# Kernel tuning notes

Measured on AMD Instinct MI355X. Metric: run time of the kernel, lower is better.

The kernel has to match this reference:

```python
import jax, jax.numpy as jnp
import numpy as np

D = 1024
H = 16
HD = D // H


def setup_inputs() -> dict:
    key = jax.random.key(0)
    ks = jax.random.split(key, 9)
    s = 1.0 / np.sqrt(D)
    return {
        "x": jax.random.normal(ks[0], (2, 2048, D), dtype=jnp.float32),
        "Wq": jax.random.normal(ks[1], (D, D), dtype=jnp.float32) * s,
        "bq": jax.random.normal(ks[2], (D,), dtype=jnp.float32) * s,
        "Wk": jax.random.normal(ks[3], (D, D), dtype=jnp.float32) * s,
        "bk": jax.random.normal(ks[4], (D,), dtype=jnp.float32) * s,
        "Wv": jax.random.normal(ks[5], (D, D), dtype=jnp.float32) * s,
        "bv": jax.random.normal(ks[6], (D,), dtype=jnp.float32) * s,
        "Wo": jax.random.normal(ks[7], (D, D), dtype=jnp.float32) * s,
        "bo": jax.random.normal(ks[8], (D,), dtype=jnp.float32) * s,
    }


def reference(x, Wq, bq, Wk, bk, Wv, bv, Wo, bo):
    B, S, _ = x.shape
    # Linear projections (torch Linear: y = x @ W.T + b)
    q = x @ Wq.T + bq
    k = x @ Wk.T + bk
    v = x @ Wv.T + bv
    # split heads: [B, S, H, HD] -> [B, H, S, HD]
    q = q.reshape(B, S, H, HD).transpose(0, 2, 1, 3)
    k = k.reshape(B, S, H, HD).transpose(0, 2, 1, 3)
    v = v.reshape(B, S, H, HD).transpose(0, 2, 1, 3)
    scale = 1.0 / jnp.sqrt(jnp.float32(HD))
    scores = jnp.einsum("bhqd,bhkd->bhqk", q, k) * scale  # [B,H,S,S]
    attn = jax.nn.softmax(scores, axis=-1)
    ctx = jnp.einsum("bhqk,bhkd->bhqd", attn, v)  # [B,H,S,HD]
    ctx = ctx.transpose(0, 2, 1, 3).reshape(B, S, D)
    out = ctx @ Wo.T + bo
    return out, attn
```

## Files before the change

### kernel.cpp

```cpp
#include <hip/hip_runtime.h>

#define S_LEN 2048
#define NH 16
#define HDIM 64
#define DMODEL 1024
#define NTOK 4096

typedef __attribute__((ext_vector_type(8))) short bf16x8;
typedef __attribute__((ext_vector_type(4))) float f32x4;

__device__ __forceinline__ unsigned short f2bf(float f) {
  union { float f; unsigned int u; } a; a.f = f;
  unsigned int u = a.u;
  u += 0x7FFFu + ((u >> 16) & 1u);
  return (unsigned short)(u >> 16);
}

__device__ __forceinline__ void gld_lds16(const unsigned short* g, unsigned short* l) {
  auto gp = (const __attribute__((address_space(1))) unsigned short*)(g);
  auto lp = (__attribute__((address_space(3))) unsigned short*)(l);
  __builtin_amdgcn_global_load_lds(gp, lp, 16, 0, 0);
}

__global__ __launch_bounds__(256) void cvt_kernel(const float* __restrict__ s,
                                                  unsigned short* __restrict__ d, int n) {
  int i = (blockIdx.x * 256 + threadIdx.x) * 4;
  if (i >= n) return;
  float4 v = *(const float4*)(s + i);
  ushort4 o;
  o.x = f2bf(v.x); o.y = f2bf(v.y); o.z = f2bf(v.z); o.w = f2bf(v.w);
  *(ushort4*)(d + i) = o;
}

__device__ __forceinline__ void gemm_core_128(
    const unsigned short* __restrict__ A, const unsigned short* __restrict__ B,
    unsigned short* Al, unsigned short* Bl, int m0, int n0, int tid, f32x4 acc[4][4])
{
  const int lane = tid & 63;
  const int wm = ((tid >> 6) >> 1) * 64;
  const int wn = ((tid >> 6) & 1) * 64;
  const int l15 = lane & 15, quad = lane >> 4;
  const int row0 = tid >> 2, c8 = (tid & 3) * 8;
  for (int kk = 0; kk < DMODEL; kk += 32) {
    gld_lds16(A + (size_t)(m0 + row0) * DMODEL + kk + c8,      Al + tid * 8);
    gld_lds16(A + (size_t)(m0 + 64 + row0) * DMODEL + kk + c8, Al + (256 + tid) * 8);
    gld_lds16(B + (size_t)(n0 + row0) * DMODEL + kk + c8,      Bl + tid * 8);
    gld_lds16(B + (size_t)(n0 + 64 + row0) * DMODEL + kk + c8, Bl + (256 + tid) * 8);
    __syncthreads();
    bf16x8 af[4], bfr[4];
#pragma unroll
    for (int i = 0; i < 4; i++) {
      af[i]  = *(const bf16x8*)(Al + (wm + i * 16 + l15) * 32 + quad * 8);
      bfr[i] = *(const bf16x8*)(Bl + (wn + i * 16 + l15) * 32 + quad * 8);
    }
#pragma unroll
    for (int i = 0; i < 4; i++)
#pragma unroll
      for (int j = 0; j < 4; j++)
        acc[i][j] = __builtin_amdgcn_mfma_f32_16x16x32_bf16(af[i], bfr[j], acc[i][j], 0, 0, 0);
    __syncthreads();
  }
}

__global__ __launch_bounds__(256) void gemm_qkv(
    const unsigned short* __restrict__ xb,
    const unsigned short* __restrict__ wq, const unsigned short* __restrict__ wk,
    const unsigned short* __restrict__ wv,
    const float* __restrict__ bq, const float* __restrict__ bk, const float* __restrict__ bv,
    unsigned short* __restrict__ q_ws, unsigned short* __restrict__ k_ws,
    unsigned short* __restrict__ vT_ws)
{
  __shared__ unsigned short Al[128 * 32];
  __shared__ unsigned short Bl[128 * 32];
  const int which = blockIdx.z;
  const unsigned short* W = which == 0 ? wq : (which == 1 ? wk : wv);
  const float* bias = which == 0 ? bq : (which == 1 ? bk : bv);
  const int m0 = blockIdx.y * 128, n0 = blockIdx.x * 128;
  const int tid = threadIdx.x, lane = tid & 63;
  const int wm = ((tid >> 6) >> 1) * 64, wn = ((tid >> 6) & 1) * 64;
  const int l15 = lane & 15, quad = lane >> 4;
  f32x4 acc[4][4] = {};
  gemm_core_128(xb, W, Al, Bl, m0, n0, tid, acc);
  const float scale = (which == 0) ? 0.125f : 1.0f;
  unsigned short* qk_dst = (which == 0) ? q_ws : k_ws;
#pragma unroll
  for (int j = 0; j < 4; j++) {
    const int n = n0 + wn + j * 16 + l15;
    const float bb = bias[n];
    const int h = n >> 6, d = n & 63;
#pragma unroll
    for (int i = 0; i < 4; i++)
#pragma unroll
      for (int r = 0; r < 4; r++) {
        const int m = m0 + wm + i * 16 + quad * 4 + r;
        const int b = m >> 11, s = m & 2047;
        const unsigned short o = f2bf((acc[i][j][r] + bb) * scale);
        if (which == 2)
          vT_ws[((size_t)(b * NH + h) * HDIM + d) * S_LEN + s] = o;
        else
          qk_dst[((size_t)(b * NH + h) * S_LEN + s) * HDIM + d] = o;
      }
  }
}

__global__ __launch_bounds__(256) void attn_fused(
    const unsigned short* __restrict__ q_ws, const unsigned short* __restrict__ k_ws,
    const unsigned short* __restrict__ vT_ws,
    float* __restrict__ attn_out, unsigned short* __restrict__ ctx_ws)
{
  __shared__ unsigned short p_lds[4][16 * 72];
  const int tid = threadIdx.x, lane = tid & 63, w = tid >> 6;
  const int l15 = lane & 15, quad = lane >> 4;
  const int bh = blockIdx.x >> 5, qtile = blockIdx.x & 31;
  const int qr0 = qtile * 64 + w * 16;

  const unsigned short* qp = q_ws + ((size_t)bh * S_LEN + qr0 + l15) * HDIM + quad * 8;
  bf16x8 aq0 = *(const bf16x8*)qp;
  bf16x8 aq1 = *(const bf16x8*)(qp + 32);

  const unsigned short* kbh = k_ws + (size_t)bh * S_LEN * HDIM;
  const unsigned short* vbh = vT_ws + (size_t)bh * HDIM * S_LEN;

  float lsum[4] = {0.f, 0.f, 0.f, 0.f};
  for (int kc = 0; kc < S_LEN; kc += 64) {
#pragma unroll
    for (int t = 0; t < 4; t++) {
      const unsigned short* kb = kbh + (size_t)(kc + t * 16 + l15) * HDIM + quad * 8;
      bf16x8 b0 = *(const bf16x8*)kb;
      bf16x8 b1 = *(const bf16x8*)(kb + 32);
      f32x4 s = {0.f, 0.f, 0.f, 0.f};
      s = __builtin_amdgcn_mfma_f32_16x16x32_bf16(aq0, b0, s, 0, 0, 0);
      s = __builtin_amdgcn_mfma_f32_16x16x32_bf16(aq1, b1, s, 0, 0, 0);
#pragma unroll
      for (int r = 0; r < 4; r++) lsum[r] += __expf(s[r]);
    }
  }
  float rinv[4];
#pragma unroll
  for (int r = 0; r < 4; r++) {
    float v = lsum[r];
    v += __shfl_xor(v, 1, 64);
    v += __shfl_xor(v, 2, 64);
    v += __shfl_xor(v, 4, 64);
    v += __shfl_xor(v, 8, 64);
    rinv[r] = 1.0f / v;
  }

  f32x4 cacc[4] = {};
  float* ab = attn_out + ((size_t)bh * S_LEN + qr0) * S_LEN;
  unsigned short* plw = &p_lds[w][0];
  for (int kc = 0; kc < S_LEN; kc += 64) {
#pragma unroll
    for (int t = 0; t < 4; t++) {
      const unsigned short* kb = kbh + (size_t)(kc + t * 16 + l15) * HDIM + quad * 8;
      bf16x8 b0 = *(const bf16x8*)kb;
      bf16x8 b1 = *(const bf16x8*)(kb + 32);
      f32x4 s = {0.f, 0.f, 0.f, 0.f};
      s = __builtin_amdgcn_mfma_f32_16x16x32_bf16(aq0, b0, s, 0, 0, 0);
      s = __builtin_amdgcn_mfma_f32_16x16x32_bf16(aq1, b1, s, 0, 0, 0);
#pragma unroll
      for (int r = 0; r < 4; r++) {
        const float p = __expf(s[r]) * rinv[r];
        ab[(size_t)(quad * 4 + r) * S_LEN + kc + t * 16 + l15] = p;
        plw[(quad * 4 + r) * 72 + t * 16 + l15] = f2bf(p);
      }
    }
    bf16x8 ap0 = *(const bf16x8*)(plw + l15 * 72 + quad * 8);
    bf16x8 ap1 = *(const bf16x8*)(plw + l15 * 72 + 32 + quad * 8);
#pragma unroll
    for (int dt = 0; dt < 4; dt++) {
      const unsigned short* vb = vbh + (size_t)(dt * 16 + l15) * S_LEN + kc + quad * 8;
      bf16x8 v0 = *(const bf16x8*)vb;
      bf16x8 v1 = *(const bf16x8*)(vb + 32);
      cacc[dt] = __builtin_amdgcn_mfma_f32_16x16x32_bf16(ap0, v0, cacc[dt], 0, 0, 0);
      cacc[dt] = __builtin_amdgcn_mfma_f32_16x16x32_bf16(ap1, v1, cacc[dt], 0, 0, 0);
    }
  }
  const int b = bh >> 4, h = bh & 15;
#pragma unroll
  for (int dt = 0; dt < 4; dt++)
#pragma unroll
    for (int r = 0; r < 4; r++) {
      const int s_ = qr0 + quad * 4 + r;
      const int d = dt * 16 + l15;
      ctx_ws[((size_t)(b * S_LEN + s_) * NH + h) * HDIM + d] = f2bf(cacc[dt][r]);
    }
}

__global__ __launch_bounds__(256) void gemm_out(
    const unsigned short* __restrict__ ctx, const unsigned short* __restrict__ wo,
    const float* __restrict__ bo, float* __restrict__ out)
{
  __shared__ unsigned short Al[128 * 32];
  __shared__ unsigned short Bl[128 * 32];
  const int m0 = blockIdx.y * 128, n0 = blockIdx.x * 128;
  const int tid = threadIdx.x, lane = tid & 63;
  const int wm = ((tid >> 6) >> 1) * 64, wn = ((tid >> 6) & 1) * 64;
  const int l15 = lane & 15, quad = lane >> 4;
  f32x4 acc[4][4] = {};
  gemm_core_128(ctx, wo, Al, Bl, m0, n0, tid, acc);
#pragma unroll
  for (int j = 0; j < 4; j++) {
    const int n = n0 + wn + j * 16 + l15;
    const float bb = bo[n];
#pragma unroll
    for (int i = 0; i < 4; i++)
#pragma unroll
      for (int r = 0; r < 4; r++) {
        const int m = m0 + wm + i * 16 + quad * 4 + r;
        out[(size_t)m * DMODEL + n] = acc[i][j][r] + bb;
      }
  }
}

extern "C" void kernel_launch(void* const* d_in, const int* in_sizes, int n_in,
                              void* d_out, int out_size, void* d_ws, size_t ws_size,
                              hipStream_t stream) {
  const float* x  = (const float*)d_in[0];
  const float* Wq = (const float*)d_in[1];
  const float* bq = (const float*)d_in[2];
  const float* Wk = (const float*)d_in[3];
  const float* bk = (const float*)d_in[4];
  const float* Wv = (const float*)d_in[5];
  const float* bv = (const float*)d_in[6];
  const float* Wo = (const float*)d_in[7];
  const float* bo = (const float*)d_in[8];

  const size_t MB = 1u << 20;
  char* ws = (char*)d_ws;
  unsigned short* xb     = (unsigned short*)(ws);
  unsigned short* wqb    = (unsigned short*)(ws + 8 * MB);
  unsigned short* wkb    = (unsigned short*)(ws + 10 * MB);
  unsigned short* wvb    = (unsigned short*)(ws + 12 * MB);
  unsigned short* wob    = (unsigned short*)(ws + 14 * MB);
  unsigned short* q_ws   = (unsigned short*)(ws + 16 * MB);
  unsigned short* k_ws   = (unsigned short*)(ws + 24 * MB);
  unsigned short* vT_ws  = (unsigned short*)(ws + 32 * MB);
  unsigned short* ctx_ws = (unsigned short*)(ws + 40 * MB);

  float* out_ptr  = (float*)d_out;
  float* attn_ptr = (float*)d_out + 4194304;

  cvt_kernel<<<4096, 256, 0, stream>>>(x,  xb,  4194304);
  cvt_kernel<<<1024, 256, 0, stream>>>(Wq, wqb, 1048576);
  cvt_kernel<<<1024, 256, 0, stream>>>(Wk, wkb, 1048576);
  cvt_kernel<<<1024, 256, 0, stream>>>(Wv, wvb, 1048576);
  cvt_kernel<<<1024, 256, 0, stream>>>(Wo, wob, 1048576);

  gemm_qkv<<<dim3(8, 32, 3), 256, 0, stream>>>(xb, wqb, wkb, wvb, bq, bk, bv,
                                               q_ws, k_ws, vT_ws);
  attn_fused<<<1024, 256, 0, stream>>>(q_ws, k_ws, vT_ws, attn_ptr, ctx_ws);
  gemm_out<<<dim3(8, 32, 1), 256, 0, stream>>>(ctx_ws, wob, bo, out_ptr);
}
```

Measured before the change: 1.015 ms.

## Split attention key range across warp pairs and vectorize probability stores

Each block now handles 32 query rows, with two waves per 16-row group, each covering half the key range. Row sums are combined through shared memory and partial context accumulators are reduced through LDS before the bf16 write. The MFMA operands are swapped so each lane holds four consecutive key columns, which allows 16-byte float4 stores of the attention matrix and packed bf16 LDS writes in place of scalar scattered stores. Twice as many blocks are launched and occupancy is hinted at 8 blocks per CU. The cost is extra synchronisation and an LDS reduction step.

```diff
diff --git a/kernel.cpp b/kernel.cpp
--- a/kernel.cpp
+++ b/kernel.cpp
@@ -103,16 +103,19 @@
   }
 }
 
-__global__ __launch_bounds__(256) void attn_fused(
+__global__ __launch_bounds__(256, 8) void attn_fused(
     const unsigned short* __restrict__ q_ws, const unsigned short* __restrict__ k_ws,
     const unsigned short* __restrict__ vT_ws,
     float* __restrict__ attn_out, unsigned short* __restrict__ ctx_ws)
 {
-  __shared__ unsigned short p_lds[4][16 * 72];
+  __shared__ __align__(16) unsigned short p_lds[4][16 * 72];
+  __shared__ float ls[4][16];
   const int tid = threadIdx.x, lane = tid & 63, w = tid >> 6;
   const int l15 = lane & 15, quad = lane >> 4;
-  const int bh = blockIdx.x >> 5, qtile = blockIdx.x & 31;
-  const int qr0 = qtile * 64 + w * 16;
+  const int rowg = w >> 1, khalf = w & 1;
+  const int bh = blockIdx.x >> 6, qt = blockIdx.x & 63;
+  const int qr0 = qt * 32 + rowg * 16;
+  const int kc0 = khalf * 1024;
 
   const unsigned short* qp = q_ws + ((size_t)bh * S_LEN + qr0 + l15) * HDIM + quad * 8;
   bf16x8 aq0 = *(const bf16x8*)qp;
@@ -121,49 +124,44 @@
   const unsigned short* kbh = k_ws + (size_t)bh * S_LEN * HDIM;
   const unsigned short* vbh = vT_ws + (size_t)bh * HDIM * S_LEN;
 
-  float lsum[4] = {0.f, 0.f, 0.f, 0.f};
-  for (int kc = 0; kc < S_LEN; kc += 64) {
+  float lsum = 0.f;
+  for (int kc = kc0; kc < kc0 + 1024; kc += 64) {
 #pragma unroll
     for (int t = 0; t < 4; t++) {
       const unsigned short* kb = kbh + (size_t)(kc + t * 16 + l15) * HDIM + quad * 8;
       bf16x8 b0 = *(const bf16x8*)kb;
       bf16x8 b1 = *(const bf16x8*)(kb + 32);
       f32x4 s = {0.f, 0.f, 0.f, 0.f};
-      s = __builtin_amdgcn_mfma_f32_16x16x32_bf16(aq0, b0, s, 0, 0, 0);
-      s = __builtin_amdgcn_mfma_f32_16x16x32_bf16(aq1, b1, s, 0, 0, 0);
-#pragma unroll
-      for (int r = 0; r < 4; r++) lsum[r] += __expf(s[r]);
-    }
-  }
-  float rinv[4];
-#pragma unroll
-  for (int r = 0; r < 4; r++) {
-    float v = lsum[r];
-    v += __shfl_xor(v, 1, 64);
-    v += __shfl_xor(v, 2, 64);
-    v += __shfl_xor(v, 4, 64);
-    v += __shfl_xor(v, 8, 64);
-    rinv[r] = 1.0f / v;
-  }
+      s = __builtin_amdgcn_mfma_f32_16x16x32_bf16(b0, aq0, s, 0, 0, 0);
+      s = __builtin_amdgcn_mfma_f32_16x16x32_bf16(b1, aq1, s, 0, 0, 0);
+      lsum += (__expf(s[0]) + __expf(s[1])) + (__expf(s[2]) + __expf(s[3]));
+    }
+  }
+  float v = lsum;
+  v += __shfl_xor(v, 16, 64);
+  v += __shfl_xor(v, 32, 64);
+  if (lane < 16) ls[w][lane] = v;
+  __syncthreads();
+  const float rinv = 1.0f / (v + ls[w ^ 1][l15]);
 
   f32x4 cacc[4] = {};
-  float* ab = attn_out + ((size_t)bh * S_LEN + qr0) * S_LEN;
+  float* abp = attn_out + ((size_t)bh * S_LEN + qr0 + l15) * S_LEN + quad * 4;
   unsigned short* plw = &p_lds[w][0];
-  for (int kc = 0; kc < S_LEN; kc += 64) {
+  for (int kc = kc0; kc < kc0 + 1024; kc += 64) {
 #pragma unroll
     for (int t = 0; t < 4; t++) {
       const unsigned short* kb = kbh + (size_t)(kc + t * 16 + l15) * HDIM + quad * 8;
       bf16x8 b0 = *(const bf16x8*)kb;
       bf16x8 b1 = *(const bf16x8*)(kb + 32);
       f32x4 s = {0.f, 0.f, 0.f, 0.f};
-      s = __builtin_amdgcn_mfma_f32_16x16x32_bf16(aq0, b0, s, 0, 0, 0);
-      s = __builtin_amdgcn_mfma_f32_16x16x32_bf16(aq1, b1, s, 0, 0, 0);
-#pragma unroll
-      for (int r = 0; r < 4; r++) {
-        const float p = __expf(s[r]) * rinv[r];
-        ab[(size_t)(quad * 4 + r) * S_LEN + kc + t * 16 + l15] = p;
-        plw[(quad * 4 + r) * 72 + t * 16 + l15] = f2bf(p);
-      }
+      s = __builtin_amdgcn_mfma_f32_16x16x32_bf16(b0, aq0, s, 0, 0, 0);
+      s = __builtin_amdgcn_mfma_f32_16x16x32_bf16(b1, aq1, s, 0, 0, 0);
+#pragma unroll
+      for (int r = 0; r < 4; r++) s[r] = __expf(s[r]) * rinv;
+      *(f32x4*)(abp + kc + t * 16) = s;
+      ushort4 pk;
+      pk.x = f2bf(s[0]); pk.y = f2bf(s[1]); pk.z = f2bf(s[2]); pk.w = f2bf(s[3]);
+      *(ushort4*)(plw + l15 * 72 + t * 16 + quad * 4) = pk;
     }
     bf16x8 ap0 = *(const bf16x8*)(plw + l15 * 72 + quad * 8);
     bf16x8 ap1 = *(const bf16x8*)(plw + l15 * 72 + 32 + quad * 8);
@@ -176,15 +174,29 @@
       cacc[dt] = __builtin_amdgcn_mfma_f32_16x16x32_bf16(ap1, v1, cacc[dt], 0, 0, 0);
     }
   }
-  const int b = bh >> 4, h = bh & 15;
-#pragma unroll
-  for (int dt = 0; dt < 4; dt++)
-#pragma unroll
-    for (int r = 0; r < 4; r++) {
-      const int s_ = qr0 + quad * 4 + r;
-      const int d = dt * 16 + l15;
-      ctx_ws[((size_t)(b * S_LEN + s_) * NH + h) * HDIM + d] = f2bf(cacc[dt][r]);
-    }
+
+  __syncthreads();
+  float* cb = (float*)&p_lds[0][0];
+  if (khalf) {
+#pragma unroll
+    for (int dt = 0; dt < 4; dt++)
+      *(f32x4*)(cb + (rowg * 64 + lane) * 16 + dt * 4) = cacc[dt];
+  }
+  __syncthreads();
+  if (!khalf) {
+#pragma unroll
+    for (int dt = 0; dt < 4; dt++)
+      cacc[dt] += *(const f32x4*)(cb + (rowg * 64 + lane) * 16 + dt * 4);
+    const int b = bh >> 4, h = bh & 15;
+#pragma unroll
+    for (int dt = 0; dt < 4; dt++)
+#pragma unroll
+      for (int r = 0; r < 4; r++) {
+        const int s_ = qr0 + quad * 4 + r;
+        const int d = dt * 16 + l15;
+        ctx_ws[((size_t)(b * S_LEN + s_) * NH + h) * HDIM + d] = f2bf(cacc[dt][r]);
+      }
+  }
 }
 
 __global__ __launch_bounds__(256) void gemm_out(
@@ -249,6 +261,6 @@
 
   gemm_qkv<<<dim3(8, 32, 3), 256, 0, stream>>>(xb, wqb, wkb, wvb, bq, bk, bv,
                                                q_ws, k_ws, vT_ws);
-  attn_fused<<<1024, 256, 0, stream>>>(q_ws, k_ws, vT_ws, attn_ptr, ctx_ws);
+  attn_fused<<<2048, 256, 0, stream>>>(q_ws, k_ws, vT_ws, attn_ptr, ctx_ws);
   gemm_out<<<dim3(8, 32, 1), 256, 0, stream>>>(ctx_ws, wob, bo, out_ptr);
 }
```

Result: no change. 1.010 ms (-0.5%).
